# Performance work log

Hardware: AMD Instinct MI355X
Metric: run time of the kernel (lower is better)

Reference implementation:

```python
import itertools
import jax, jax.numpy as jnp
import numpy as np

GRID = 16384      # self.shape = (GRID,)
LAYERS = 8        # num_layers
SPAN = 2          # span = (2,)
K = 2 * SPAN + 1  # kernel size = 5 (ninputs)
NPOS = 2 ** K     # 32 possible boolean input combos
BATCH = 32
M = 4096          # x width; GRID % M == 0
STRIDE = GRID // M

# bitmask: all 2^K boolean input combinations, shape (NPOS, K)
_BITMASK = jnp.asarray(list(itertools.product(range(2), repeat=K)), dtype=jnp.float32)


def setup_inputs() -> dict:
    key = jax.random.key(0)
    k1, k2 = jax.random.split(key)
    x = jax.random.uniform(k1, (BATCH, M), dtype=jnp.float32)
    toggle_gates = jax.random.uniform(k2, (LAYERS, NPOS, GRID), dtype=jnp.float32)
    return {"x": x, "toggle_gates": toggle_gates}


def _convolve(state):
    # torch convolve(): offsets 0..K-1 via wrap-around roll, then spatial roll by
    # -SPAN to center the window -> neighbor n+i-SPAN (mod GRID) at kernel idx i.
    # jnp.roll(state, SPAN - i) gives out[:, n] = state[:, n + i - SPAN mod GRID].
    return jnp.stack([jnp.roll(state, SPAN - i, axis=1) for i in range(K)], axis=-1)  # (B, N, K)


def reference(x, toggle_gates):
    tw = jax.nn.sigmoid(toggle_gates)  # (L, NPOS, N)
    # embed(): scatter x evenly into the grid, rest is scratch (zeros)
    state = jnp.zeros((x.shape[0], GRID), dtype=x.dtype).at[:, ::STRIDE].set(x)

    def step(s, tw_layer):
        conv = _convolve(s)  # (B, N, K)
        # weight[c, b, n] = prod_i (1 - |bitmask[c, i] - conv[b, n, i]|)
        w = jnp.prod(1.0 - jnp.abs(_BITMASK[:, None, None, :] - conv[None]), axis=-1)  # (C, B, N)
        new = jnp.clip(jnp.einsum('cbn,cn->bn', w, tw_layer), 0.0, 1.0)
        return new, None

    state, _ = jax.lax.scan(step, state, tw)
    # forward returns state[slices] = state[:, ::STRIDE]
    return state[:, ::STRIDE]
```

## Files before the change

### kernel.cpp

```cpp
#include <hip/hip_runtime.h>

#define GRID_N 16384
#define NLAYERS 8
#define NPOS 32
#define BATCH 32
#define MW 4096
#define TILE 32
#define HALO 16
#define WBUF 64
#define ROWP 36

typedef float f2 __attribute__((ext_vector_type(2)));

__device__ __forceinline__ float dpp_shr1(float v) {
    return __builtin_bit_cast(float, __builtin_amdgcn_update_dpp(
        0, __builtin_bit_cast(int, v), 0x138, 0xF, 0xF, true));
}
__device__ __forceinline__ float dpp_shl1(float v) {
    return __builtin_bit_cast(float, __builtin_amdgcn_update_dpp(
        0, __builtin_bit_cast(int, v), 0x130, 0xF, 0xF, true));
}
__device__ __forceinline__ f2 shr1(f2 v) { f2 r; r.x = dpp_shr1(v.x); r.y = dpp_shr1(v.y); return r; }
__device__ __forceinline__ f2 shl1(f2 v) { f2 r; r.x = dpp_shl1(v.x); r.y = dpp_shl1(v.y); return r; }

__device__ __forceinline__ float sigm(float v) {
    return __builtin_amdgcn_rcpf(1.0f + __expf(-v));
}

__global__ __launch_bounds__(512, 4) void ASIC_44186623541335_kernel(
    const float* __restrict__ x,
    const float* __restrict__ tg,
    float* __restrict__ out)
{
    __shared__ __align__(16) float twl[2][WBUF][ROWP];

    const int tid = threadIdx.x;
    const int tx  = tid & 63;
    const int w   = tid >> 6;
    const int c0  = 4 * w;
    const int start = blockIdx.x * TILE;
    const int gcol  = (start - HALO + tx) & (GRID_N - 1);

    float pf[8];
    #pragma unroll
    for (int ll = 0; ll < 2; ++ll)
        #pragma unroll
        for (int k = 0; k < 4; ++k)
            pf[ll * 4 + k] = tg[((size_t)ll * NPOS + c0 + k) * GRID_N + gcol];

    f2 S[2];
    {
        const bool on = (gcol & 3) == 0;
        const int  m  = gcol >> 2;
        #pragma unroll
        for (int q = 0; q < 2; ++q) {
            f2 v = {0.0f, 0.0f};
            if (on) {
                v.x = x[(c0 + 2 * q)     * MW + m];
                v.y = x[(c0 + 2 * q + 1) * MW + m];
            }
            S[q] = v;
        }
    }

    #pragma unroll
    for (int ll = 0; ll < 2; ++ll) {
        float4 sg;
        sg.x = sigm(pf[ll * 4 + 0]);
        sg.y = sigm(pf[ll * 4 + 1]);
        sg.z = sigm(pf[ll * 4 + 2]);
        sg.w = sigm(pf[ll * 4 + 3]);
        *(float4*)&twl[ll][tx][c0] = sg;
    }
    #pragma unroll
    for (int ll = 0; ll < 2; ++ll)
        #pragma unroll
        for (int k = 0; k < 4; ++k)
            pf[ll * 4 + k] = tg[((size_t)(2 + ll) * NPOS + c0 + k) * GRID_N + gcol];
    __syncthreads();

    #pragma unroll
    for (int g = 0; g < 4; ++g) {
        #pragma unroll
        for (int ll = 0; ll < 2; ++ll) {
            f2 s0v[2], s1v[2], s3v[2], s4v[2];
            #pragma unroll
            for (int q = 0; q < 2; ++q) {
                s1v[q] = shr1(S[q]);
                s0v[q] = shr1(s1v[q]);
                s3v[q] = shl1(S[q]);
                s4v[q] = shl1(s3v[q]);
            }

            f2 u0[16], u1[16];
            #pragma unroll
            for (int k = 0; k < 8; ++k) {
                const float4 t4 = *(const float4*)&twl[ll][tx][4 * k];
                const float dA = t4.y - t4.x;
                const float dB = t4.w - t4.z;
                u0[2 * k]     = __builtin_elementwise_fma(s4v[0], (f2)dA, (f2)t4.x);
                u0[2 * k + 1] = __builtin_elementwise_fma(s4v[0], (f2)dB, (f2)t4.z);
                u1[2 * k]     = __builtin_elementwise_fma(s4v[1], (f2)dA, (f2)t4.x);
                u1[2 * k + 1] = __builtin_elementwise_fma(s4v[1], (f2)dB, (f2)t4.z);
            }

            #pragma unroll
            for (int q = 0; q < 2; ++q) {
                f2* u = q ? u1 : u0;
                #pragma unroll
                for (int r = 0; r < 8; ++r)
                    u[r] = __builtin_elementwise_fma(s3v[q], u[2 * r + 1] - u[2 * r], u[2 * r]);
                #pragma unroll
                for (int r = 0; r < 4; ++r)
                    u[r] = __builtin_elementwise_fma(S[q],   u[2 * r + 1] - u[2 * r], u[2 * r]);
                #pragma unroll
                for (int r = 0; r < 2; ++r)
                    u[r] = __builtin_elementwise_fma(s1v[q], u[2 * r + 1] - u[2 * r], u[2 * r]);
                f2 rv = __builtin_elementwise_fma(s0v[q], u[1] - u[0], u[0]);
                rv = __builtin_elementwise_min(__builtin_elementwise_max(rv, (f2)0.0f), (f2)1.0f);
                S[q] = rv;
            }
        }

        if (g < 3) {
            __syncthreads();
            #pragma unroll
            for (int ll = 0; ll < 2; ++ll) {
                float4 sg;
                sg.x = sigm(pf[ll * 4 + 0]);
                sg.y = sigm(pf[ll * 4 + 1]);
                sg.z = sigm(pf[ll * 4 + 2]);
                sg.w = sigm(pf[ll * 4 + 3]);
                *(float4*)&twl[ll][tx][c0] = sg;
            }
            if (g < 2) {
                const float* tn = tg + (size_t)(2 * g + 4) * NPOS * GRID_N;
                #pragma unroll
                for (int ll = 0; ll < 2; ++ll)
                    #pragma unroll
                    for (int k = 0; k < 4; ++k)
                        pf[ll * 4 + k] = tn[((size_t)ll * NPOS + c0 + k) * GRID_N + gcol];
            }
            __syncthreads();
        }
    }

    const int rel = tx - HALO;
    if (rel >= 0 && rel < TILE && (rel & 3) == 0) {
        const int m = (start >> 2) + (rel >> 2);
        out[(c0 + 0) * MW + m] = S[0].x;
        out[(c0 + 1) * MW + m] = S[0].y;
        out[(c0 + 2) * MW + m] = S[1].x;
        out[(c0 + 3) * MW + m] = S[1].y;
    }
}

extern "C" void kernel_launch(void* const* d_in, const int* in_sizes, int n_in,
                              void* d_out, int out_size, void* d_ws, size_t ws_size,
                              hipStream_t stream) {
    const float* x  = (const float*)d_in[0];
    const float* tg = (const float*)d_in[1];
    float* out = (float*)d_out;
    ASIC_44186623541335_kernel<<<GRID_N / TILE, 512, 0, stream>>>(x, tg, out);
}
```

Before: 78.91 us.

## Prefetch all eight layers' gates upfront and stage four layers per LDS buffer

Issues all 32 per-thread gate loads (all 8 layers) at kernel start instead of double-buffering two layers at a time, and doubles the LDS buffer to hold four layers so only one mid-kernel refill and barrier pair is needed. The aim is to expose all global memory latency at once and cut synchronization points from three refills to one. The layer loop is also no longer fully unrolled. The cost is more registers (pf grows from 8 to 32) and twice the shared memory per block, which may reduce occupancy under the 512x4 launch bounds.

Result: slower. 80.97 us (+2.6%).

```diff
diff --git a/kernel.cpp b/kernel.cpp
--- a/kernel.cpp
+++ b/kernel.cpp
@@ -32,7 +32,7 @@
     const float* __restrict__ tg,
     float* __restrict__ out)
 {
-    __shared__ __align__(16) float twl[2][WBUF][ROWP];
+    __shared__ __align__(16) float twl[4][WBUF][ROWP];
 
     const int tid = threadIdx.x;
     const int tx  = tid & 63;
@@ -41,12 +41,12 @@
     const int start = blockIdx.x * TILE;
     const int gcol  = (start - HALO + tx) & (GRID_N - 1);
 
-    float pf[8];
+    float pf[32];
     #pragma unroll
-    for (int ll = 0; ll < 2; ++ll)
+    for (int l = 0; l < NLAYERS; ++l)
         #pragma unroll
         for (int k = 0; k < 4; ++k)
-            pf[ll * 4 + k] = tg[((size_t)ll * NPOS + c0 + k) * GRID_N + gcol];
+            pf[l * 4 + k] = tg[((size_t)l * NPOS + c0 + k) * GRID_N + gcol];
 
     f2 S[2];
     {
@@ -64,82 +64,65 @@
     }
 
     #pragma unroll
-    for (int ll = 0; ll < 2; ++ll) {
+    for (int l4 = 0; l4 < 4; ++l4) {
         float4 sg;
-        sg.x = sigm(pf[ll * 4 + 0]);
-        sg.y = sigm(pf[ll * 4 + 1]);
-        sg.z = sigm(pf[ll * 4 + 2]);
-        sg.w = sigm(pf[ll * 4 + 3]);
-        *(float4*)&twl[ll][tx][c0] = sg;
+        sg.x = sigm(pf[l4 * 4 + 0]);
+        sg.y = sigm(pf[l4 * 4 + 1]);
+        sg.z = sigm(pf[l4 * 4 + 2]);
+        sg.w = sigm(pf[l4 * 4 + 3]);
+        *(float4*)&twl[l4][tx][c0] = sg;
     }
-    #pragma unroll
-    for (int ll = 0; ll < 2; ++ll)
-        #pragma unroll
-        for (int k = 0; k < 4; ++k)
-            pf[ll * 4 + k] = tg[((size_t)(2 + ll) * NPOS + c0 + k) * GRID_N + gcol];
     __syncthreads();
 
-    #pragma unroll
-    for (int g = 0; g < 4; ++g) {
+    for (int l = 0; l < NLAYERS; ++l) {
+        f2 s0v[2], s1v[2], s3v[2], s4v[2];
         #pragma unroll
-        for (int ll = 0; ll < 2; ++ll) {
-            f2 s0v[2], s1v[2], s3v[2], s4v[2];
-            #pragma unroll
-            for (int q = 0; q < 2; ++q) {
-                s1v[q] = shr1(S[q]);
-                s0v[q] = shr1(s1v[q]);
-                s3v[q] = shl1(S[q]);
-                s4v[q] = shl1(s3v[q]);
-            }
-
-            f2 u0[16], u1[16];
-            #pragma unroll
-            for (int k = 0; k < 8; ++k) {
-                const float4 t4 = *(const float4*)&twl[ll][tx][4 * k];
-                const float dA = t4.y - t4.x;
-                const float dB = t4.w - t4.z;
-                u0[2 * k]     = __builtin_elementwise_fma(s4v[0], (f2)dA, (f2)t4.x);
-                u0[2 * k + 1] = __builtin_elementwise_fma(s4v[0], (f2)dB, (f2)t4.z);
-                u1[2 * k]     = __builtin_elementwise_fma(s4v[1], (f2)dA, (f2)t4.x);
-                u1[2 * k + 1] = __builtin_elementwise_fma(s4v[1], (f2)dB, (f2)t4.z);
-            }
-
-            #pragma unroll
-            for (int q = 0; q < 2; ++q) {
-                f2* u = q ? u1 : u0;
-                #pragma unroll
-                for (int r = 0; r < 8; ++r)
-                    u[r] = __builtin_elementwise_fma(s3v[q], u[2 * r + 1] - u[2 * r], u[2 * r]);
-                #pragma unroll
-                for (int r = 0; r < 4; ++r)
-                    u[r] = __builtin_elementwise_fma(S[q],   u[2 * r + 1] - u[2 * r], u[2 * r]);
-                #pragma unroll
-                for (int r = 0; r < 2; ++r)
-                    u[r] = __builtin_elementwise_fma(s1v[q], u[2 * r + 1] - u[2 * r], u[2 * r]);
-                f2 rv = __builtin_elementwise_fma(s0v[q], u[1] - u[0], u[0]);
-                rv = __builtin_elementwise_min(__builtin_elementwise_max(rv, (f2)0.0f), (f2)1.0f);
-                S[q] = rv;
-            }
+        for (int q = 0; q < 2; ++q) {
+            s1v[q] = shr1(S[q]);
+            s0v[q] = shr1(s1v[q]);
+            s3v[q] = shl1(S[q]);
+            s4v[q] = shl1(s3v[q]);
         }
 
-        if (g < 3) {
+        f2 u0[16], u1[16];
+        #pragma unroll
+        for (int k = 0; k < 8; ++k) {
+            const float4 t4 = *(const float4*)&twl[l & 3][tx][4 * k];
+            const float dA = t4.y - t4.x;
+            const float dB = t4.w - t4.z;
+            u0[2 * k]     = __builtin_elementwise_fma(s4v[0], (f2)dA, (f2)t4.x);
+            u0[2 * k + 1] = __builtin_elementwise_fma(s4v[0], (f2)dB, (f2)t4.z);
+            u1[2 * k]     = __builtin_elementwise_fma(s4v[1], (f2)dA, (f2)t4.x);
+            u1[2 * k + 1] = __builtin_elementwise_fma(s4v[1], (f2)dB, (f2)t4.z);
+        }
+
+        #pragma unroll
+        for (int q = 0; q < 2; ++q) {
+            f2* u = q ? u1 : u0;
+            #pragma unroll
+            for (int r = 0; r < 8; ++r)
+                u[r] = __builtin_elementwise_fma(s3v[q], u[2 * r + 1] - u[2 * r], u[2 * r]);
+            #pragma unroll
+            for (int r = 0; r < 4; ++r)
+                u[r] = __builtin_elementwise_fma(S[q],   u[2 * r + 1] - u[2 * r], u[2 * r]);
+            #pragma unroll
+            for (int r = 0; r < 2; ++r)
+                u[r] = __builtin_elementwise_fma(s1v[q], u[2 * r + 1] - u[2 * r], u[2 * r]);
+            f2 rv = __builtin_elementwise_fma(s0v[q], u[1] - u[0], u[0]);
+            rv = __builtin_elementwise_min(__builtin_elementwise_max(rv, (f2)0.0f), (f2)1.0f);
+            S[q] = rv;
+        }
+
+        if (l == 3) {
             __syncthreads();
             #pragma unroll
-            for (int ll = 0; ll < 2; ++ll) {
+            for (int l4 = 0; l4 < 4; ++l4) {
                 float4 sg;
-                sg.x = sigm(pf[ll * 4 + 0]);
-                sg.y = sigm(pf[ll * 4 + 1]);
-                sg.z = sigm(pf[ll * 4 + 2]);
-                sg.w = sigm(pf[ll * 4 + 3]);
-                *(float4*)&twl[ll][tx][c0] = sg;
-            }
-            if (g < 2) {
-                const float* tn = tg + (size_t)(2 * g + 4) * NPOS * GRID_N;
-                #pragma unroll
-                for (int ll = 0; ll < 2; ++ll)
-                    #pragma unroll
-                    for (int k = 0; k < 4; ++k)
-                        pf[ll * 4 + k] = tn[((size_t)ll * NPOS + c0 + k) * GRID_N + gcol];
+                sg.x = sigm(pf[16 + l4 * 4 + 0]);
+                sg.y = sigm(pf[16 + l4 * 4 + 1]);
+                sg.z = sigm(pf[16 + l4 * 4 + 2]);
+                sg.w = sigm(pf[16 + l4 * 4 + 3]);
+                *(float4*)&twl[l4][tx][c0] = sg;
             }
             __syncthreads();
         }
```
